# Kernel optimization log

Measured on AMD Instinct MI355X. Metric: run time of the kernel, lower is better.

Reference implementation:

```python
import jax, jax.numpy as jnp
import numpy as np
from jax import lax

VOCAB = 400000
D = 300          # embedding_dim
L = 2000         # seq len
B = 4            # batch
C1, K1 = 64, 3   # conv1 outChan, kernel
C2, K2 = 128, 500
HID = 256
NCLS = 5


def setup_inputs() -> dict:
    key = jax.random.key(0)
    ks = jax.random.split(key, 8)
    x = jax.random.randint(ks[0], (B, L), 0, VOCAB)
    emb_table = jax.random.normal(ks[1], (VOCAB, D), jnp.float32) * 0.1
    conv1_w = jax.random.normal(ks[2], (C1, 1, K1), jnp.float32) * 0.1
    conv1_b = jnp.zeros((C1,), jnp.float32)
    conv2_w = jax.random.normal(ks[3], (C2, C1, K2), jnp.float32) * 0.02
    conv2_b = jnp.zeros((C2,), jnp.float32)
    lin1_w = jax.random.normal(ks[4], (HID, C2), jnp.float32) * 0.05
    lin1_b = jnp.zeros((HID,), jnp.float32)
    lin2_w = jax.random.normal(ks[5], (NCLS, HID), jnp.float32) * 0.05
    lin2_b = jnp.zeros((NCLS,), jnp.float32)
    return dict(x=x, emb_table=emb_table,
                conv1_w=conv1_w, conv1_b=conv1_b,
                conv2_w=conv2_w, conv2_b=conv2_b,
                lin1_w=lin1_w, lin1_b=lin1_b,
                lin2_w=lin2_w, lin2_b=lin2_b)


def _conv1d(x, w):
    # x: [N, Cin, W]; w: [Cout, Cin, K]; VALID, stride 1
    return lax.conv_general_dilated(x, w, window_strides=(1,), padding='VALID',
                                    dimension_numbers=('NCH', 'OIH', 'NCH'))


def _maxpool1d(x, k):
    # kernel == stride (torch MaxPool1d default)
    return lax.reduce_window(x, -jnp.inf, lax.max, (1, 1, k), (1, 1, k), 'VALID')


def reference(x, emb_table, conv1_w, conv1_b, conv2_w, conv2_b,
              lin1_w, lin1_b, lin2_w, lin2_b):
    emb = emb_table[x]                                  # [B, L, D]
    # concat module == reshape to [B, 1, L*D]
    out = emb.reshape(emb.shape[0], 1, emb.shape[1] * emb.shape[2])
    out = _conv1d(out, conv1_w) + conv1_b[None, :, None]  # [B, C1, L*D-K1+1]
    out = _maxpool1d(jax.nn.relu(out), D)                 # pool 300
    out = _conv1d(out, conv2_w) + conv2_b[None, :, None]  # [B, C2, 1500]
    out = _maxpool1d(jax.nn.relu(out), D * 5)             # pool 1500 -> len 1
    out = out.reshape(out.shape[0], -1)                   # [B, C2]
    out = jax.nn.relu(out @ lin1_w.T + lin1_b)            # [B, HID]
    out = jax.nn.softmax(out @ lin2_w.T + lin2_b, axis=-1)  # [B, 5]
    # Dropout is identity in eval mode
    return out
```

## Files before the change

### kernel.cpp

```cpp
#include <hip/hip_runtime.h>
#include <hip/hip_bf16.h>
#include <math.h>

#define VOCAB 400000
#define D     300
#define L     2000
#define B     4
#define C1    64
#define C2    128
#define K2    500
#define HID   256
#define NCLS  5
#define NP1   1999
#define T2    1500
#define T2P   1536
#define TPAD  2304
#define S     8
#define CI    8
#define NK2   125
#define BN    96
#define SEGR  640
#define NWT   128
#define NC1B  (B * 500)

typedef __attribute__((ext_vector_type(8))) short short8v;
typedef __attribute__((ext_vector_type(4))) float f32x4;

__device__ __forceinline__ void gload_lds16(const void* g, void* l) {
    __builtin_amdgcn_global_load_lds(
        (const __attribute__((address_space(1))) void*)g,
        (__attribute__((address_space(3))) void*)l, 16, 0, 0);
}

__global__ __launch_bounds__(256) void k_prep(
    const int* __restrict__ x, const float* __restrict__ emb,
    const float* __restrict__ w1, const float* __restrict__ b1,
    const float* __restrict__ w2,
    __hip_bfloat16* __restrict__ in1T, __hip_bfloat16* __restrict__ aT)
{
    __shared__ float smem[1204];
    int bid = blockIdx.x, tid = threadIdx.x;
    if (bid < NWT) {
        int s = bid >> 4, cog = bid & 15;
        for (int u = tid; u < 4000; u += 256) {
            int co_l = u & 7, kg = u >> 3;
            int k2 = kg >> 2, g = kg & 3;
            int co = cog * 8 + co_l;
            __hip_bfloat16 tmp[8];
#pragma unroll
            for (int e = 0; e < 8; ++e)
                tmp[e] = __float2bfloat16(
                    w2[((size_t)co * C1 + s * CI + e) * K2 + 4 * k2 + g]);
            *reinterpret_cast<int4*>(
                aT + ((size_t)((s * NK2 + k2) * 4 + g)) * 1024 + (size_t)co * 8) =
                *reinterpret_cast<const int4*>(tmp);
        }
    } else {
        int blk = bid - NWT;
        int b = blk / 500, pb = blk % 500;
        int p0 = pb * 4;
        float* sig = smem;
        for (int i = tid; i < 301; i += 256) {
            int rj = i / 75, col = (i % 75) * 4;
            int xi = p0 + rj; if (xi > L - 1) xi = L - 1;
            int row = x[b * L + xi];
            *reinterpret_cast<float4*>(sig + 4 * i) =
                *reinterpret_cast<const float4*>(emb + (size_t)row * D + col);
        }
        __syncthreads();
        int c = tid & 63, pg = tid >> 6;
        int p = p0 + pg;
        float wa = w1[c * 3 + 0], wb = w1[c * 3 + 1], wc = w1[c * 3 + 2];
        float bb = b1[c];
        int jb = 300 * pg;
        float m = -INFINITY;
        float4 cur = *reinterpret_cast<float4*>(sig + jb);
        for (int st = 0; st < 75; ++st) {
            float4 nxt = *reinterpret_cast<float4*>(sig + jb + 4 * st + 4);
            float xx[8] = {cur.x, cur.y, cur.z, cur.w, nxt.x, nxt.y, nxt.z, nxt.w};
#pragma unroll
            for (int q = 0; q < 4; ++q) {
                float v = fmaf(wc, xx[q + 2], fmaf(wb, xx[q + 1], fmaf(wa, xx[q], bb)));
                m = fmaxf(m, v);
            }
            cur = nxt;
        }
        if (p < NP1) {
            int sg = c >> 3, ci = c & 7;
            in1T[((size_t)(b * S + sg) * TPAD + p) * CI + ci] =
                __float2bfloat16(fmaxf(m, 0.0f));
        }
    }
}

__global__ __launch_bounds__(256, 2) void k2_mfma(
    const __hip_bfloat16* __restrict__ in1T,
    const __hip_bfloat16* __restrict__ aT,
    __hip_bfloat16* __restrict__ part)
{
    int bid = blockIdx.x;
    int s = bid & 7;
    int rem = bid >> 3;
    int b = rem >> 4, ti = rem & 15;
    int t0 = ti * BN;

    __shared__ __align__(16) __hip_bfloat16 seg[SEGR * CI];

    int tid = threadIdx.x;
    int w = tid >> 6, l = tid & 63;
    int lane16 = l & 15, g = l >> 4;
    int co0w = (w & 1) * 64;
    int tn0  = (w >> 1) * 48;

    {
        const char* gsrc = (const char*)(in1T + ((size_t)(b * S + s) * TPAD + t0) * CI);
        char* lb = (char*)seg + w * 1024;
        gload_lds16(gsrc + (size_t)tid * 16, lb);
        gload_lds16(gsrc + (size_t)(256 + tid) * 16, lb + 4096);
        if (tid < 128)
            gload_lds16(gsrc + (size_t)(512 + tid) * 16, lb + 8192);
    }
    __syncthreads();

    const __hip_bfloat16* abase =
        aT + (size_t)s * NK2 * 4096 + g * 1024 + (co0w + lane16) * 8;

    f32x4 acc[4][3];
#pragma unroll
    for (int fa = 0; fa < 4; ++fa)
#pragma unroll
        for (int fb = 0; fb < 3; ++fb) acc[fa][fb] = (f32x4){0.f, 0.f, 0.f, 0.f};

#define LOADA(AR, KK)                                                         \
    {                                                                         \
        _Pragma("unroll")                                                     \
        for (int fa = 0; fa < 4; ++fa)                                        \
            AR[fa] = *reinterpret_cast<const short8v*>(                       \
                abase + (size_t)(KK) * 4096 + fa * 128);                      \
    }

#define STEP(AR, KK)                                                         \
    {                                                                         \
        short8v bfr[3];                                                       \
        _Pragma("unroll")                                                     \
        for (int fb = 0; fb < 3; ++fb)                                        \
            bfr[fb] = *reinterpret_cast<const short8v*>(                      \
                seg + (size_t)(tn0 + fb * 16 + lane16 + 4 * (KK) + g) * 8);   \
        __builtin_amdgcn_s_setprio(1);                                        \
        _Pragma("unroll")                                                     \
        for (int fa = 0; fa < 4; ++fa) {                                      \
            _Pragma("unroll")                                                 \
            for (int fb = 0; fb < 3; ++fb)                                    \
                acc[fa][fb] = __builtin_amdgcn_mfma_f32_16x16x32_bf16(        \
                    AR[fa], bfr[fb], acc[fa][fb], 0, 0, 0);                   \
        }                                                                     \
        __builtin_amdgcn_s_setprio(0);                                        \
    }

    short8v a0[4], a1[4];
    LOADA(a0, 0);
    LOADA(a1, 1);
    int k2 = 0;
#pragma unroll 1
    for (; k2 + 3 < NK2; k2 += 2) {
        STEP(a0, k2);
        LOADA(a0, k2 + 2);
        STEP(a1, k2 + 1);
        LOADA(a1, k2 + 3);
    }
    STEP(a0, k2);
    LOADA(a0, k2 + 2);
    STEP(a1, k2 + 1);
    STEP(a0, k2 + 2);

#undef LOADA
#undef STEP

#pragma unroll
    for (int fa = 0; fa < 4; ++fa) {
#pragma unroll
        for (int fb = 0; fb < 3; ++fb) {
            int t = t0 + tn0 + fb * 16 + lane16;
            int cob = co0w + fa * 16 + 4 * g;
#pragma unroll
            for (int r = 0; r < 4; ++r) {
                float v = (t < T2) ? acc[fa][fb][r] : -INFINITY;
                part[((size_t)(s * B + b) * C2 + cob + r) * T2P + t] =
                    __float2bfloat16(v);
            }
        }
    }
}

__global__ __launch_bounds__(256) void k2b_pool(
    const __hip_bfloat16* __restrict__ part, const float* __restrict__ b2,
    float* __restrict__ h1)
{
    int bc = blockIdx.x;
    int b = bc / C2, co = bc % C2;
    int tid = threadIdx.x;
    float m = -INFINITY;
    if (tid < 192) {
        int t8 = tid * 8;
        float sum[8] = {0.f, 0.f, 0.f, 0.f, 0.f, 0.f, 0.f, 0.f};
#pragma unroll
        for (int s = 0; s < S; ++s) {
            short8v v = *reinterpret_cast<const short8v*>(
                part + ((size_t)(s * B + b) * C2 + co) * T2P + t8);
#pragma unroll
            for (int e = 0; e < 8; ++e)
                sum[e] += __uint_as_float(((unsigned)(unsigned short)v[e]) << 16);
        }
#pragma unroll
        for (int e = 0; e < 8; ++e) m = fmaxf(m, sum[e]);
    }
    __shared__ float red[256];
    red[tid] = m;
    __syncthreads();
    for (int st = 128; st > 0; st >>= 1) {
        if (tid < st) red[tid] = fmaxf(red[tid], red[tid + st]);
        __syncthreads();
    }
    if (tid == 0) h1[bc] = fmaxf(red[0] + b2[co], 0.0f);
}

__global__ __launch_bounds__(256) void k3_head(
    const float* __restrict__ h1,
    const float* __restrict__ wl1, const float* __restrict__ bl1,
    const float* __restrict__ wl2, const float* __restrict__ bl2,
    float* __restrict__ out)
{
    int b = blockIdx.x;
    int tid = threadIdx.x;
    __shared__ float xin[C2];
    __shared__ float hbuf[HID];
    __shared__ float lg[NCLS];
    if (tid < C2) xin[tid] = h1[b * C2 + tid];
    __syncthreads();
    float a = bl1[tid];
    for (int c = 0; c < C2; ++c) a = fmaf(xin[c], wl1[tid * C2 + c], a);
    hbuf[tid] = fmaxf(a, 0.0f);
    __syncthreads();
    if (tid < NCLS) {
        float lv = bl2[tid];
        for (int j = 0; j < HID; ++j) lv = fmaf(hbuf[j], wl2[tid * HID + j], lv);
        lg[tid] = lv;
    }
    __syncthreads();
    if (tid < NCLS) {
        float mx = lg[0];
        for (int i = 1; i < NCLS; ++i) mx = fmaxf(mx, lg[i]);
        float sum = 0.f;
        for (int i = 0; i < NCLS; ++i) sum += expf(lg[i] - mx);
        out[b * NCLS + tid] = expf(lg[tid] - mx) / sum;
    }
}

extern "C" void kernel_launch(void* const* d_in, const int* in_sizes, int n_in,
                              void* d_out, int out_size, void* d_ws, size_t ws_size,
                              hipStream_t stream)
{
    const int*   x   = (const int*)  d_in[0];
    const float* emb = (const float*)d_in[1];
    const float* w1  = (const float*)d_in[2];
    const float* b1  = (const float*)d_in[3];
    const float* w2  = (const float*)d_in[4];
    const float* b2  = (const float*)d_in[5];
    const float* wl1 = (const float*)d_in[6];
    const float* bl1 = (const float*)d_in[7];
    const float* wl2 = (const float*)d_in[8];
    const float* bl2 = (const float*)d_in[9];
    float* out = (float*)d_out;

    __hip_bfloat16* part = (__hip_bfloat16*)d_ws;
    float* h1 = (float*)(part + (size_t)S * B * C2 * T2P);
    __hip_bfloat16* in1T = (__hip_bfloat16*)(h1 + 512);
    __hip_bfloat16* aT   = in1T + (size_t)B * S * TPAD * CI;

    hipLaunchKernelGGL(k_prep, dim3(NWT + NC1B), dim3(256), 0, stream,
                       x, emb, w1, b1, w2, in1T, aT);
    hipLaunchKernelGGL(k2_mfma, dim3(512), dim3(256), 0, stream, in1T, aT, part);
    hipLaunchKernelGGL(k2b_pool, dim3(B * C2), dim3(256), 0, stream, part, b2, h1);
    hipLaunchKernelGGL(k3_head, dim3(B), dim3(256), 0, stream,
                       h1, wl1, bl1, wl2, bl2, out);
}
```

Before: 74.57 us.

## Switch conv2 GEMM to 32x32x16 MFMA with retiled co/time blocking

Replaces the 16x16x32 bf16 MFMA tiling in the conv2 kernel with 32x32x16 MFMAs. The weight layout becomes 16-wide k groups in halves. The block tile changes from 128 channels by 96 time steps to 64 channels by 192 time steps, with a channel-group grid dimension. A-fragment loads drop to one vector per step with a four-deep register prefetch ring. The aim is fewer MFMA issues and A loads per FLOP, at the cost of doubling the number of k steps and changing the per-block LDS segment and grid shape.

```diff
diff --git a/kernel.cpp b/kernel.cpp
--- a/kernel.cpp
+++ b/kernel.cpp
@@ -17,14 +17,14 @@
 #define TPAD  2304
 #define S     8
 #define CI    8
-#define NK2   125
-#define BN    96
-#define SEGR  640
+#define NK16  250
+#define BN    192
+#define SEGR  704
 #define NWT   128
 #define NC1B  (B * 500)
 
 typedef __attribute__((ext_vector_type(8))) short short8v;
-typedef __attribute__((ext_vector_type(4))) float f32x4;
+typedef __attribute__((ext_vector_type(16))) float f32x16;
 
 __device__ __forceinline__ void gload_lds16(const void* g, void* l) {
     __builtin_amdgcn_global_load_lds(
@@ -44,15 +44,15 @@
         int s = bid >> 4, cog = bid & 15;
         for (int u = tid; u < 4000; u += 256) {
             int co_l = u & 7, kg = u >> 3;
-            int k2 = kg >> 2, g = kg & 3;
+            int k2 = kg >> 1, h = kg & 1;
             int co = cog * 8 + co_l;
             __hip_bfloat16 tmp[8];
 #pragma unroll
             for (int e = 0; e < 8; ++e)
                 tmp[e] = __float2bfloat16(
-                    w2[((size_t)co * C1 + s * CI + e) * K2 + 4 * k2 + g]);
+                    w2[((size_t)co * C1 + s * CI + e) * K2 + kg]);
             *reinterpret_cast<int4*>(
-                aT + ((size_t)((s * NK2 + k2) * 4 + g)) * 1024 + (size_t)co * 8) =
+                aT + ((size_t)((s * NK16 + k2) * 2 + h)) * 1024 + (size_t)co * 8) =
                 *reinterpret_cast<const int4*>(tmp);
         }
     } else {
@@ -101,93 +101,85 @@
     int bid = blockIdx.x;
     int s = bid & 7;
     int rem = bid >> 3;
-    int b = rem >> 4, ti = rem & 15;
+    int ti = rem & 7;
+    int b  = (rem >> 3) & 3;
+    int cog = rem >> 5;
     int t0 = ti * BN;
 
     __shared__ __align__(16) __hip_bfloat16 seg[SEGR * CI];
 
     int tid = threadIdx.x;
     int w = tid >> 6, l = tid & 63;
-    int lane16 = l & 15, g = l >> 4;
-    int co0w = (w & 1) * 64;
-    int tn0  = (w >> 1) * 48;
+    int l32 = l & 31, h = l >> 5;
+    int co0w = cog * 64 + (w & 1) * 32;
+    int tn0  = (w >> 1) * 96;
 
     {
         const char* gsrc = (const char*)(in1T + ((size_t)(b * S + s) * TPAD + t0) * CI);
         char* lb = (char*)seg + w * 1024;
         gload_lds16(gsrc + (size_t)tid * 16, lb);
         gload_lds16(gsrc + (size_t)(256 + tid) * 16, lb + 4096);
-        if (tid < 128)
+        if (tid < 192)
             gload_lds16(gsrc + (size_t)(512 + tid) * 16, lb + 8192);
     }
     __syncthreads();
 
     const __hip_bfloat16* abase =
-        aT + (size_t)s * NK2 * 4096 + g * 1024 + (co0w + lane16) * 8;
-
-    f32x4 acc[4][3];
-#pragma unroll
-    for (int fa = 0; fa < 4; ++fa)
-#pragma unroll
-        for (int fb = 0; fb < 3; ++fb) acc[fa][fb] = (f32x4){0.f, 0.f, 0.f, 0.f};
+        aT + (size_t)s * NK16 * 2048 + h * 1024 + (co0w + l32) * 8;
+
+    f32x16 acc[3];
+#pragma unroll
+    for (int fb = 0; fb < 3; ++fb)
+#pragma unroll
+        for (int r = 0; r < 16; ++r) acc[fb][r] = 0.f;
 
 #define LOADA(AR, KK)                                                         \
-    {                                                                         \
-        _Pragma("unroll")                                                     \
-        for (int fa = 0; fa < 4; ++fa)                                        \
-            AR[fa] = *reinterpret_cast<const short8v*>(                       \
-                abase + (size_t)(KK) * 4096 + fa * 128);                      \
-    }
-
-#define STEP(AR, KK)                                                         \
+    AR = *reinterpret_cast<const short8v*>(abase + (size_t)(KK) * 2048);
+
+#define STEP(AR, KK)                                                          \
     {                                                                         \
         short8v bfr[3];                                                       \
         _Pragma("unroll")                                                     \
         for (int fb = 0; fb < 3; ++fb)                                        \
             bfr[fb] = *reinterpret_cast<const short8v*>(                      \
-                seg + (size_t)(tn0 + fb * 16 + lane16 + 4 * (KK) + g) * 8);   \
+                seg + (size_t)(tn0 + fb * 32 + l32 + 2 * (KK) + h) * 8);      \
         __builtin_amdgcn_s_setprio(1);                                        \
         _Pragma("unroll")                                                     \
-        for (int fa = 0; fa < 4; ++fa) {                                      \
-            _Pragma("unroll")                                                 \
-            for (int fb = 0; fb < 3; ++fb)                                    \
-                acc[fa][fb] = __builtin_amdgcn_mfma_f32_16x16x32_bf16(        \
-                    AR[fa], bfr[fb], acc[fa][fb], 0, 0, 0);                   \
-        }                                                                     \
+        for (int fb = 0; fb < 3; ++fb)                                        \
+            acc[fb] = __builtin_amdgcn_mfma_f32_32x32x16_bf16(                \
+                AR, bfr[fb], acc[fb], 0, 0, 0);                               \
         __builtin_amdgcn_s_setprio(0);                                        \
     }
 
-    short8v a0[4], a1[4];
-    LOADA(a0, 0);
-    LOADA(a1, 1);
+    short8v a0, a1, a2, a3;
+    LOADA(a0, 0); LOADA(a1, 1); LOADA(a2, 2); LOADA(a3, 3);
     int k2 = 0;
 #pragma unroll 1
-    for (; k2 + 3 < NK2; k2 += 2) {
-        STEP(a0, k2);
-        LOADA(a0, k2 + 2);
-        STEP(a1, k2 + 1);
-        LOADA(a1, k2 + 3);
-    }
-    STEP(a0, k2);
-    LOADA(a0, k2 + 2);
-    STEP(a1, k2 + 1);
-    STEP(a0, k2 + 2);
+    for (; k2 + 7 < NK16; k2 += 4) {
+        STEP(a0, k2);     LOADA(a0, k2 + 4);
+        STEP(a1, k2 + 1); LOADA(a1, k2 + 5);
+        STEP(a2, k2 + 2); LOADA(a2, k2 + 6);
+        STEP(a3, k2 + 3); LOADA(a3, k2 + 7);
+    }
+    STEP(a0, 244); LOADA(a0, 248);
+    STEP(a1, 245); LOADA(a1, 249);
+    STEP(a2, 246);
+    STEP(a3, 247);
+    STEP(a0, 248);
+    STEP(a1, 249);
 
 #undef LOADA
 #undef STEP
 
 #pragma unroll
-    for (int fa = 0; fa < 4; ++fa) {
-#pragma unroll
-        for (int fb = 0; fb < 3; ++fb) {
-            int t = t0 + tn0 + fb * 16 + lane16;
-            int cob = co0w + fa * 16 + 4 * g;
-#pragma unroll
-            for (int r = 0; r < 4; ++r) {
-                float v = (t < T2) ? acc[fa][fb][r] : -INFINITY;
-                part[((size_t)(s * B + b) * C2 + cob + r) * T2P + t] =
-                    __float2bfloat16(v);
-            }
+    for (int fb = 0; fb < 3; ++fb) {
+        int t = t0 + tn0 + fb * 32 + l32;
+#pragma unroll
+        for (int r = 0; r < 16; ++r) {
+            int row = (r & 3) + 8 * (r >> 2) + 4 * h;
+            float v = (t < T2) ? acc[fb][r] : -INFINITY;
+            part[((size_t)(s * B + b) * C2 + co0w + row) * T2P + t] =
+                __float2bfloat16(v);
         }
     }
 }
```

Result: slower. 77.55 us (+4.0%).
